# Performance work log

Hardware: AMD Instinct MI355X
Metric: run time of the kernel (lower is better)

Reference implementation:

```python
import jax, jax.numpy as jnp
import numpy as np

B, L, H, NUM_LABELS = 4, 256, 768, 13


def setup_inputs() -> dict:
    key = jax.random.key(0)
    k1, k2, k3, k4, k5 = jax.random.split(key, 5)
    s1 = 1.0 / np.sqrt(2 * H)
    s2 = 1.0 / np.sqrt(H)
    return {
        "hidden_states": jax.random.normal(k1, (B, L, H), dtype=jnp.float32),
        "W1": jax.random.uniform(k2, (2 * H, H), jnp.float32, -s1, s1),
        "b1": jax.random.uniform(k3, (H,), jnp.float32, -s1, s1),
        "W2": jax.random.uniform(k4, (H, NUM_LABELS), jnp.float32, -s2, s2),
        "b2": jax.random.uniform(k5, (NUM_LABELS,), jnp.float32, -s2, s2),
    }


def reference(hidden_states, W1, b1, W2, b2):
    # Original: ffn(cat([x_start expand over dim2, x_end expand over dim1], -1))
    # Algebraically: Linear(2H->H) on the concat == proj(x_start) + proj(x_end)
    # broadcast over the L x L span grid, avoiding the (B,L,L,2H) tensor.
    H_ = hidden_states.shape[-1]
    xs_proj = jnp.einsum('bsh,hk->bsk', hidden_states, W1[:H_])   # start half
    xe_proj = jnp.einsum('bsh,hk->bsk', hidden_states, W1[H_:])   # end half
    h = xs_proj[:, :, None, :] + xe_proj[:, None, :, :] + b1      # (B,L,L,H)
    h = jax.nn.gelu(h, approximate=False)                         # torch GELU default = exact erf
    logits = jnp.einsum('bijk,kn->bijn', h, W2) + b2              # (B,L,L,num_labels)
    return logits
```

## Files before the change

### kernel.cpp

```cpp
#include <hip/hip_runtime.h>
#include <math.h>

#define H 768
#define L 256
#define NB 4
#define NL 13

typedef _Float16 h2 __attribute__((ext_vector_type(2)));
typedef _Float16 h4 __attribute__((ext_vector_type(4)));
typedef _Float16 half8 __attribute__((ext_vector_type(8)));
typedef float f32x4 __attribute__((ext_vector_type(4)));

__device__ inline h2 gelu_pk(h2 x) {
    const _Float16 kC = (_Float16)3.75f;
    h2 hi = {kC, kC}, lo = {(_Float16)-3.75f, (_Float16)-3.75f};
    h2 xc = __builtin_elementwise_min(__builtin_elementwise_max(x, lo), hi);
    h2 u = xc * xc;
    const _Float16 d4v = (_Float16)2.0333e-5f,  d3v = (_Float16)-0.00084672f;
    const _Float16 d2v = (_Float16)0.0140002f,  d1v = (_Float16)-0.1234557f;
    const _Float16 d0v = (_Float16)0.7946463f;
    h2 d4 = {d4v, d4v}, d3 = {d3v, d3v}, d2 = {d2v, d2v}, d1 = {d1v, d1v}, d0 = {d0v, d0v};
    h2 p = u * (u * (u * (u * d4 + d3) + d2) + d1) + d0;
    h2 t = xc * p;
    h2 w = x * t + x;
    const _Float16 kH = (_Float16)0.5f;
    h2 halfv = {kH, kH};
    return w * halfv;
}

__global__ __launch_bounds__(256) void gemm_fused(
    const float* __restrict__ X, const float* __restrict__ W1,
    const float* __restrict__ b1, const float* __restrict__ W2,
    _Float16* __restrict__ Pxs2, _Float16* __restrict__ Pxe,
    _Float16* __restrict__ Bfrag2)
{
    const int tid = threadIdx.x;

    if (blockIdx.x >= 768) {
        int base = (blockIdx.x - 768) * 768 + tid;
        #pragma unroll
        for (int r = 0; r < 3; ++r) {
            int idx = base + r * 256;
            int u = idx & 7;
            int lane = (idx >> 3) & 63;
            int kb = idx >> 9;
            int k = kb * 32 + ((lane >> 4) << 3) + u;
            int nn = lane & 15;
            float v = (nn < NL) ? W2[(size_t)k * NL + nn] : 0.f;
            Bfrag2[idx] = (_Float16)v;
        }
        return;
    }

    __shared__ _Float16 As[2][32][72];
    __shared__ _Float16 Bs[2][64][72];

    const int w = tid >> 6, lane = tid & 63;
    const int ln = lane & 15, quad = lane >> 4;
    const int bm = blockIdx.x & 31;
    const int bn = blockIdx.x >> 5;
    const int m0 = bm * 32;
    const int n0g = bn * 64;
    const bool isE = (n0g >= H);
    const float* Wb = W1 + (isE ? (size_t)H * H : 0);
    const int c0 = isE ? (n0g - H) : n0g;

    const int ar = tid >> 4;
    const int ac = (tid & 15) * 4;

    float4 fA0, fA1, fB0a, fB0b, fB1a, fB1b;

#define G_LOAD(KR) do { \
    const int k0_ = (KR) * 64; \
    fA0 = *(const float4*)&X[(size_t)(m0 + ar) * H + k0_ + ac]; \
    fA1 = *(const float4*)&X[(size_t)(m0 + 16 + ar) * H + k0_ + ac]; \
    const float* wr0_ = &Wb[(size_t)(k0_ + 2 * ar) * H + c0 + ac]; \
    fB0a = *(const float4*)wr0_; \
    fB0b = *(const float4*)(wr0_ + H); \
    const float* wr1_ = &Wb[(size_t)(k0_ + 2 * (16 + ar)) * H + c0 + ac]; \
    fB1a = *(const float4*)wr1_; \
    fB1b = *(const float4*)(wr1_ + H); \
} while (0)

#define L_STORE(BUF) do { \
    h4 oa0 = { (_Float16)fA0.x, (_Float16)fA0.y, (_Float16)fA0.z, (_Float16)fA0.w }; \
    h4 oa1 = { (_Float16)fA1.x, (_Float16)fA1.y, (_Float16)fA1.z, (_Float16)fA1.w }; \
    *(h4*)&As[BUF][ar][ac] = oa0; \
    *(h4*)&As[BUF][16 + ar][ac] = oa1; \
    h2 p0 = {(_Float16)fB0a.x, (_Float16)fB0b.x}; \
    h2 p1 = {(_Float16)fB0a.y, (_Float16)fB0b.y}; \
    h2 p2 = {(_Float16)fB0a.z, (_Float16)fB0b.z}; \
    h2 p3 = {(_Float16)fB0a.w, (_Float16)fB0b.w}; \
    *(h2*)&Bs[BUF][ac + 0][2 * ar] = p0; \
    *(h2*)&Bs[BUF][ac + 1][2 * ar] = p1; \
    *(h2*)&Bs[BUF][ac + 2][2 * ar] = p2; \
    *(h2*)&Bs[BUF][ac + 3][2 * ar] = p3; \
    h2 q0 = {(_Float16)fB1a.x, (_Float16)fB1b.x}; \
    h2 q1 = {(_Float16)fB1a.y, (_Float16)fB1b.y}; \
    h2 q2 = {(_Float16)fB1a.z, (_Float16)fB1b.z}; \
    h2 q3 = {(_Float16)fB1a.w, (_Float16)fB1b.w}; \
    *(h2*)&Bs[BUF][ac + 0][2 * (16 + ar)] = q0; \
    *(h2*)&Bs[BUF][ac + 1][2 * (16 + ar)] = q1; \
    *(h2*)&Bs[BUF][ac + 2][2 * (16 + ar)] = q2; \
    *(h2*)&Bs[BUF][ac + 3][2 * (16 + ar)] = q3; \
} while (0)

    const int wm = w & 1, wn = w >> 1;
    f32x4 acc[2] = {};

    G_LOAD(0);
    L_STORE(0);
    __syncthreads();

    for (int kr = 0; kr < 12; ++kr) {
        const int cur = kr & 1;
        if (kr < 11) G_LOAD(kr + 1);
        #pragma unroll
        for (int sub = 0; sub < 2; ++sub) {
            const int ko = sub * 32 + quad * 8;
            half8 a   = *(const half8*)&As[cur][wm * 16 + ln][ko];
            half8 b0  = *(const half8*)&Bs[cur][wn * 32 + ln][ko];
            half8 b1f = *(const half8*)&Bs[cur][wn * 32 + 16 + ln][ko];
            acc[0] = __builtin_amdgcn_mfma_f32_16x16x32_f16(a, b0,  acc[0], 0, 0, 0);
            acc[1] = __builtin_amdgcn_mfma_f32_16x16x32_f16(a, b1f, acc[1], 0, 0, 0);
        }
        if (kr < 11) L_STORE(cur ^ 1);
        __syncthreads();
    }

    const int mb = m0 + wm * 16 + quad * 4;
    const int nb = wn * 32;
    if (!isE) {
        float bv0 = b1[n0g + nb + ln];
        float bv1 = b1[n0g + nb + 16 + ln];
        #pragma unroll
        for (int r = 0; r < 4; ++r) {
            Pxs2[(size_t)(mb + r) * H + (n0g + nb + ln)]      = (_Float16)(acc[0][r] + bv0);
            Pxs2[(size_t)(mb + r) * H + (n0g + nb + 16 + ln)] = (_Float16)(acc[1][r] + bv1);
        }
    } else {
        #pragma unroll
        for (int r = 0; r < 4; ++r) {
            Pxe[(size_t)(mb + r) * H + (c0 + nb + ln)]      = (_Float16)acc[0][r];
            Pxe[(size_t)(mb + r) * H + (c0 + nb + 16 + ln)] = (_Float16)acc[1][r];
        }
    }
#undef G_LOAD
#undef L_STORE
}

__global__ __launch_bounds__(256, 6) void span_mfma_kernel(
    const _Float16* __restrict__ Pxs2, const _Float16* __restrict__ Pxe,
    const _Float16* __restrict__ Bfrag2, const float* __restrict__ b2,
    float* __restrict__ out)
{
    __shared__ unsigned int xsf[4 * H / 2];
    __shared__ f32x4 redbuf[2][4][64];
    const int ip = blockIdx.x >> 3;
    const int jq = blockIdx.x & 7;
    const int bi0 = ip * 4;
    const int b = bi0 >> 8;
    const int tid = threadIdx.x;

    const unsigned int* xsrc = (const unsigned int*)(Pxs2 + (size_t)bi0 * H);
    #pragma unroll
    for (int t = 0; t < 6; ++t) xsf[t * 256 + tid] = xsrc[t * 256 + tid];

    const int w = tid >> 6;
    const int lane = tid & 63;
    const int jh = w & 1;
    const int kh = w >> 1;
    const int n = lane & 15;
    const int quad = lane >> 4;
    const int j_load = jq * 32 + jh * 16 + n;

    const int kb0 = kh * 12;
    const int kbe = kb0 + 12;

    const _Float16* xerow = Pxe + (size_t)(b * L + j_load) * H + quad * 8;
    const half8* bptr = (const half8*)(Bfrag2 + (size_t)lane * 8);

    f32x4 acc[4] = {};
    __syncthreads();

    uint4 xe0 = *(const uint4*)(xerow + kb0 * 32);
    uint4 xe1 = *(const uint4*)(xerow + (kb0 + 1) * 32);
    uint4 bf0 = *(const uint4*)(bptr + (size_t)kb0 * 64);
    uint4 bf1 = *(const uint4*)(bptr + (size_t)(kb0 + 1) * 64);

    #pragma unroll 3
    for (int kb = kb0; kb < kbe; ++kb) {
        uint4 xecur = xe0;  xe0 = xe1;
        uint4 bfcur = bf0;  bf0 = bf1;
        if (kb + 2 < kbe) {
            xe1 = *(const uint4*)(xerow + (kb + 2) * 32);
            bf1 = *(const uint4*)(bptr + (size_t)(kb + 2) * 64);
        }

        half8 bfrag = __builtin_bit_cast(half8, bfcur);
        h2 xep[4] = { __builtin_bit_cast(h2, xecur.x), __builtin_bit_cast(h2, xecur.y),
                      __builtin_bit_cast(h2, xecur.z), __builtin_bit_cast(h2, xecur.w) };
        const int xo = kb * 16 + quad * 4;

        #pragma unroll
        for (int i01 = 0; i01 < 4; ++i01) {
            uint4 xsd = *(const uint4*)&xsf[i01 * (H / 2) + xo];
            h2 xsp[4] = { __builtin_bit_cast(h2, xsd.x), __builtin_bit_cast(h2, xsd.y),
                          __builtin_bit_cast(h2, xsd.z), __builtin_bit_cast(h2, xsd.w) };
            unsigned int pk[4];
            #pragma unroll
            for (int p = 0; p < 4; ++p) {
                h2 g = gelu_pk(xsp[p] + xep[p]);
                pk[p] = __builtin_bit_cast(unsigned int, g);
            }
            uint4 pk4 = {pk[0], pk[1], pk[2], pk[3]};
            half8 afrag = __builtin_bit_cast(half8, pk4);
            acc[i01] = __builtin_amdgcn_mfma_f32_16x16x32_f16(afrag, bfrag, acc[i01], 0, 0, 0);
        }
    }

    if (kh == 1) {
        #pragma unroll
        for (int i01 = 0; i01 < 4; ++i01) redbuf[jh][i01][lane] = acc[i01];
    }
    __syncthreads();

    if (kh == 0 && n < NL) {
        float b2v = b2[n];
        #pragma unroll
        for (int i01 = 0; i01 < 4; ++i01) {
            f32x4 r2 = redbuf[jh][i01][lane];
            #pragma unroll
            for (int r = 0; r < 4; ++r) {
                int j = jq * 32 + jh * 16 + quad * 4 + r;
                out[((size_t)(bi0 + i01) * L + j) * NL + n] = acc[i01][r] + r2[r] + b2v;
            }
        }
    }
}

extern "C" void kernel_launch(void* const* d_in, const int* in_sizes, int n_in,
                              void* d_out, int out_size, void* d_ws, size_t ws_size,
                              hipStream_t stream)
{
    (void)in_sizes; (void)n_in; (void)out_size; (void)ws_size;
    const float* X  = (const float*)d_in[0];
    const float* W1 = (const float*)d_in[1];
    const float* b1 = (const float*)d_in[2];
    const float* W2 = (const float*)d_in[3];
    const float* b2 = (const float*)d_in[4];
    float* out = (float*)d_out;

    char* ws = (char*)d_ws;
    _Float16* Pxs2   = (_Float16*)ws;
    _Float16* Pxe    = Pxs2 + (size_t)NB * L * H;
    _Float16* Bfrag2 = Pxe + (size_t)NB * L * H;

    gemm_fused<<<dim3(784), 256, 0, stream>>>(X, W1, b1, W2, Pxs2, Pxe, Bfrag2);
    span_mfma_kernel<<<dim3(2048), 256, 0, stream>>>(Pxs2, Pxe, Bfrag2, b2, out);
}
```

Before: 123.6 us.

## Drop split-K in span kernel, widen j tile, and hand-code packed GELU asm

Each wave now covers the full K range (24 k-blocks) for its own 16 j columns, and each block covers 64 j. This removes the LDS reduction buffer, the extra barrier, and half the redundant xs staging, and halves the grid to 1024 blocks. The packed-FP16 GELU polynomial becomes inline asm, with its constants held in registers and pinned through an empty asm. The trade is fewer blocks and waves for latency hiding, plus a lower occupancy hint in launch_bounds.

```diff
diff --git a/kernel.cpp b/kernel.cpp
--- a/kernel.cpp
+++ b/kernel.cpp
@@ -11,21 +11,34 @@
 typedef _Float16 half8 __attribute__((ext_vector_type(8)));
 typedef float f32x4 __attribute__((ext_vector_type(4)));
 
-__device__ inline h2 gelu_pk(h2 x) {
-    const _Float16 kC = (_Float16)3.75f;
-    h2 hi = {kC, kC}, lo = {(_Float16)-3.75f, (_Float16)-3.75f};
-    h2 xc = __builtin_elementwise_min(__builtin_elementwise_max(x, lo), hi);
-    h2 u = xc * xc;
-    const _Float16 d4v = (_Float16)2.0333e-5f,  d3v = (_Float16)-0.00084672f;
-    const _Float16 d2v = (_Float16)0.0140002f,  d1v = (_Float16)-0.1234557f;
-    const _Float16 d0v = (_Float16)0.7946463f;
-    h2 d4 = {d4v, d4v}, d3 = {d3v, d3v}, d2 = {d2v, d2v}, d1 = {d1v, d1v}, d0 = {d0v, d0v};
-    h2 p = u * (u * (u * (u * d4 + d3) + d2) + d1) + d0;
-    h2 t = xc * p;
-    h2 w = x * t + x;
-    const _Float16 kH = (_Float16)0.5f;
-    h2 halfv = {kH, kH};
-    return w * halfv;
+__device__ inline unsigned int gelu_asm(
+    unsigned int xs, unsigned int xe,
+    unsigned int lo, unsigned int hi,
+    unsigned int d4, unsigned int d3, unsigned int d2, unsigned int d1,
+    unsigned int d0, unsigned int hf)
+{
+    unsigned int x, xc, u, p;
+    asm("v_pk_add_f16 %0, %4, %5\n\t"
+        "v_pk_max_f16 %1, %0, %6\n\t"
+        "v_pk_min_f16 %1, %1, %7\n\t"
+        "v_pk_mul_f16 %2, %1, %1\n\t"
+        "v_pk_fma_f16 %3, %2, %8, %9\n\t"
+        "v_pk_fma_f16 %3, %2, %3, %10\n\t"
+        "v_pk_fma_f16 %3, %2, %3, %11\n\t"
+        "v_pk_fma_f16 %3, %2, %3, %12\n\t"
+        "v_pk_mul_f16 %3, %1, %3\n\t"
+        "v_pk_fma_f16 %3, %0, %3, %0\n\t"
+        "v_pk_mul_f16 %0, %3, %13"
+        : "=&v"(x), "=&v"(xc), "=&v"(u), "=&v"(p)
+        : "v"(xs), "v"(xe), "v"(lo), "v"(hi), "v"(d4), "v"(d3),
+          "v"(d2), "v"(d1), "v"(d0), "v"(hf));
+    return x;
+}
+
+__device__ inline unsigned int h2const(float f) {
+    _Float16 c = (_Float16)f;
+    h2 r = {c, c};
+    return __builtin_bit_cast(unsigned int, r);
 }
 
 __global__ __launch_bounds__(256) void gemm_fused(
@@ -149,15 +162,14 @@
 #undef L_STORE
 }
 
-__global__ __launch_bounds__(256, 6) void span_mfma_kernel(
+__global__ __launch_bounds__(256, 4) void span_mfma_kernel(
     const _Float16* __restrict__ Pxs2, const _Float16* __restrict__ Pxe,
     const _Float16* __restrict__ Bfrag2, const float* __restrict__ b2,
     float* __restrict__ out)
 {
     __shared__ unsigned int xsf[4 * H / 2];
-    __shared__ f32x4 redbuf[2][4][64];
-    const int ip = blockIdx.x >> 3;
-    const int jq = blockIdx.x & 7;
+    const int ip = blockIdx.x >> 2;
+    const int jq = blockIdx.x & 3;
     const int bi0 = ip * 4;
     const int b = bi0 >> 8;
     const int tid = threadIdx.x;
@@ -166,76 +178,64 @@
     #pragma unroll
     for (int t = 0; t < 6; ++t) xsf[t * 256 + tid] = xsrc[t * 256 + tid];
 
-    const int w = tid >> 6;
+    const int wave = tid >> 6;
     const int lane = tid & 63;
-    const int jh = w & 1;
-    const int kh = w >> 1;
     const int n = lane & 15;
     const int quad = lane >> 4;
-    const int j_load = jq * 32 + jh * 16 + n;
-
-    const int kb0 = kh * 12;
-    const int kbe = kb0 + 12;
+    const int j_load = jq * 64 + wave * 16 + n;
 
     const _Float16* xerow = Pxe + (size_t)(b * L + j_load) * H + quad * 8;
-    const half8* bptr = (const half8*)(Bfrag2 + (size_t)lane * 8);
+    const uint4* bptr = (const uint4*)(Bfrag2 + (size_t)lane * 8);
+
+    unsigned int cLo = h2const(-3.75f), cHi = h2const(3.75f);
+    unsigned int cD4 = h2const(2.0333e-5f), cD3 = h2const(-0.00084672f);
+    unsigned int cD2 = h2const(0.0140002f), cD1 = h2const(-0.1234557f);
+    unsigned int cD0 = h2const(0.7946463f), cHf = h2const(0.5f);
+    asm("" : "+v"(cLo), "+v"(cHi), "+v"(cD4), "+v"(cD3),
+             "+v"(cD2), "+v"(cD1), "+v"(cD0), "+v"(cHf));
 
     f32x4 acc[4] = {};
     __syncthreads();
 
-    uint4 xe0 = *(const uint4*)(xerow + kb0 * 32);
-    uint4 xe1 = *(const uint4*)(xerow + (kb0 + 1) * 32);
-    uint4 bf0 = *(const uint4*)(bptr + (size_t)kb0 * 64);
-    uint4 bf1 = *(const uint4*)(bptr + (size_t)(kb0 + 1) * 64);
-
-    #pragma unroll 3
-    for (int kb = kb0; kb < kbe; ++kb) {
+    uint4 xe0 = *(const uint4*)(xerow);
+    uint4 xe1 = *(const uint4*)(xerow + 32);
+    uint4 bf0 = bptr[0];
+    uint4 bf1 = bptr[64];
+
+    #pragma unroll 4
+    for (int kb = 0; kb < H / 32; ++kb) {
         uint4 xecur = xe0;  xe0 = xe1;
         uint4 bfcur = bf0;  bf0 = bf1;
-        if (kb + 2 < kbe) {
+        if (kb < H / 32 - 2) {
             xe1 = *(const uint4*)(xerow + (kb + 2) * 32);
-            bf1 = *(const uint4*)(bptr + (size_t)(kb + 2) * 64);
+            bf1 = bptr[(kb + 2) * 64];
         }
 
         half8 bfrag = __builtin_bit_cast(half8, bfcur);
-        h2 xep[4] = { __builtin_bit_cast(h2, xecur.x), __builtin_bit_cast(h2, xecur.y),
-                      __builtin_bit_cast(h2, xecur.z), __builtin_bit_cast(h2, xecur.w) };
         const int xo = kb * 16 + quad * 4;
 
         #pragma unroll
         for (int i01 = 0; i01 < 4; ++i01) {
             uint4 xsd = *(const uint4*)&xsf[i01 * (H / 2) + xo];
-            h2 xsp[4] = { __builtin_bit_cast(h2, xsd.x), __builtin_bit_cast(h2, xsd.y),
-                          __builtin_bit_cast(h2, xsd.z), __builtin_bit_cast(h2, xsd.w) };
-            unsigned int pk[4];
-            #pragma unroll
-            for (int p = 0; p < 4; ++p) {
-                h2 g = gelu_pk(xsp[p] + xep[p]);
-                pk[p] = __builtin_bit_cast(unsigned int, g);
-            }
-            uint4 pk4 = {pk[0], pk[1], pk[2], pk[3]};
+            unsigned int pk0 = gelu_asm(xsd.x, xecur.x, cLo, cHi, cD4, cD3, cD2, cD1, cD0, cHf);
+            unsigned int pk1 = gelu_asm(xsd.y, xecur.y, cLo, cHi, cD4, cD3, cD2, cD1, cD0, cHf);
+            unsigned int pk2 = gelu_asm(xsd.z, xecur.z, cLo, cHi, cD4, cD3, cD2, cD1, cD0, cHf);
+            unsigned int pk3 = gelu_asm(xsd.w, xecur.w, cLo, cHi, cD4, cD3, cD2, cD1, cD0, cHf);
+            uint4 pk4 = {pk0, pk1, pk2, pk3};
             half8 afrag = __builtin_bit_cast(half8, pk4);
             acc[i01] = __builtin_amdgcn_mfma_f32_16x16x32_f16(afrag, bfrag, acc[i01], 0, 0, 0);
         }
     }
 
-    if (kh == 1) {
-        #pragma unroll
-        for (int i01 = 0; i01 < 4; ++i01) redbuf[jh][i01][lane] = acc[i01];
-    }
-    __syncthreads();
-
-    if (kh == 0 && n < NL) {
+    if (n < NL) {
         float b2v = b2[n];
         #pragma unroll
-        for (int i01 = 0; i01 < 4; ++i01) {
-            f32x4 r2 = redbuf[jh][i01][lane];
+        for (int i01 = 0; i01 < 4; ++i01)
             #pragma unroll
             for (int r = 0; r < 4; ++r) {
-                int j = jq * 32 + jh * 16 + quad * 4 + r;
-                out[((size_t)(bi0 + i01) * L + j) * NL + n] = acc[i01][r] + r2[r] + b2v;
+                int j = jq * 64 + wave * 16 + quad * 4 + r;
+                out[((size_t)(bi0 + i01) * L + j) * NL + n] = acc[i01][r] + b2v;
             }
-        }
     }
 }
 
@@ -257,5 +257,5 @@
     _Float16* Bfrag2 = Pxe + (size_t)NB * L * H;
 
     gemm_fused<<<dim3(784), 256, 0, stream>>>(X, W1, b1, W2, Pxs2, Pxe, Bfrag2);
-    span_mfma_kernel<<<dim3(2048), 256, 0, stream>>>(Pxs2, Pxe, Bfrag2, b2, out);
-}
+    span_mfma_kernel<<<NB * L, 256, 0, stream>>>(Pxs2, Pxe, Bfrag2, b2, out);
+}
```

After: 123.2 us. No clear change (-0.3%).
